# Kernel optimization log

Measured on AMD Instinct MI355X. Metric: run time of the kernel, lower is better.

Reference implementation:

```python
import jax, jax.numpy as jnp
import numpy as np

B, L, D, H, VOCAB = 8, 1024, 1024, 8, 32000
DH = D // H  # dim_per_head = 128
SCALE = float((DH // H) ** (-0.5))  # faithful to key.size(-1)//num_heads
EPS = 1e-5


def setup_inputs() -> dict:
    key = jax.random.key(0)
    ks = jax.random.split(key, 12)
    tokens = jax.random.randint(ks[0], (B, L), 0, VOCAB)
    s = 0.02
    emb = jax.random.normal(ks[1], (VOCAB, D), jnp.float32) * s
    emb = emb.at[0].set(0.0)  # padding_idx=0
    Wq = jax.random.normal(ks[2], (D, D), jnp.float32) * s
    Wk = jax.random.normal(ks[3], (D, D), jnp.float32) * s
    Wv = jax.random.normal(ks[4], (D, D), jnp.float32) * s
    Wo = jax.random.normal(ks[5], (D, D), jnp.float32) * s
    bq = jnp.zeros((D,), jnp.float32)
    bk = jnp.zeros((D,), jnp.float32)
    bv = jnp.zeros((D,), jnp.float32)
    bo = jnp.zeros((D,), jnp.float32)
    gamma = jnp.ones((2 * D,), jnp.float32)
    beta = jnp.zeros((2 * D,), jnp.float32)
    return {"tokens": tokens, "emb": emb, "Wq": Wq, "bq": bq, "Wk": Wk,
            "bk": bk, "Wv": Wv, "bv": bv, "Wo": Wo, "bo": bo,
            "gamma": gamma, "beta": beta}


def reference(tokens, emb, Wq, bq, Wk, bk, Wv, bv, Wo, bo, gamma, beta):
    # padding mask: [B, L, L] True where key token == 0
    pad = (tokens == 0)  # [B, L]
    mask = jnp.broadcast_to(pad[:, None, :], (B, L, L))
    mask = jnp.tile(mask, (H, 1, 1))  # torch .repeat(num_heads,1,1) -> [H*B, L, L]

    x = emb[tokens]  # [B, L, D]

    q = (x @ Wq + bq).reshape(B * H, L, DH)  # faithful interleaved view
    k = (x @ Wk + bk).reshape(B * H, L, DH)
    v = (x @ Wv + bv).reshape(B * H, L, DH)

    scores = jnp.einsum('bqd,bkd->bqk', q, k) * SCALE
    scores = jnp.where(mask, -jnp.inf, scores)
    attn = jax.nn.softmax(scores, axis=-1)
    ctx = jnp.einsum('bqk,bkd->bqd', attn, v).reshape(B, L, D)

    out = ctx @ Wo + bo  # [B, L, D]
    r = x + out
    maxpool = r.max(axis=1)   # [B, D]
    meanpool = r.mean(axis=1)  # [B, D]
    agg = jnp.concatenate([maxpool, meanpool], axis=1)  # [B, 2D]

    mu = agg.mean(axis=-1, keepdims=True)
    var = agg.var(axis=-1, keepdims=True)
    return (agg - mu) / jnp.sqrt(var + EPS) * gamma + beta
```

## Files before the change

### kernel.cpp

```cpp
#include <hip/hip_runtime.h>
#include <math.h>

typedef __attribute__((ext_vector_type(8))) short short8;
typedef __attribute__((ext_vector_type(4))) float f32x4;

constexpr int CB = 8, CL = 1024, CD = 1024, CDH = 128, CM = 8192;
constexpr float CSCALE = 0.25f;
constexpr float CEPS = 1e-5f;

__device__ inline ushort f2b(float f) {
    union { float f; unsigned u; } v; v.f = f;
    unsigned r = v.u + 0x7FFF + ((v.u >> 16) & 1);
    return (ushort)(r >> 16);
}

__device__ inline void gld16(const void* g, void* l) {
    __builtin_amdgcn_global_load_lds(
        (const __attribute__((address_space(1))) void*)g,
        (__attribute__((address_space(3))) void*)l, 16, 0, 0);
}

__global__ __launch_bounds__(256) void k_gather(const int* __restrict__ tokens,
                                                const float* __restrict__ emb,
                                                float* __restrict__ x,
                                                ushort* __restrict__ xb) {
    int row = blockIdx.x;
    int tok = tokens[row];
    float4 v = ((const float4*)(emb + (size_t)tok * CD))[threadIdx.x];
    ((float4*)(x + (size_t)row * CD))[threadIdx.x] = v;
    ushort4 o; o.x = f2b(v.x); o.y = f2b(v.y); o.z = f2b(v.z); o.w = f2b(v.w);
    ((ushort4*)(xb + (size_t)row * CD))[threadIdx.x] = o;
}

__global__ __launch_bounds__(256) void k_wtrans(const float* __restrict__ W,
                                                ushort* __restrict__ Wt) {
    __shared__ float ws_[32][33];
    const int tk = blockIdx.x * 32, tn = blockIdx.y * 32;
    const int t = threadIdx.x;
    {
        int r = t >> 3, c4 = (t & 7) * 4;
        *(float4*)&ws_[r][c4] = *(const float4*)&W[(size_t)(tk + r) * CD + tn + c4];
    }
    __syncthreads();
    int n = t >> 3, k4 = (t & 7) * 4;
    ushort4 o;
    o.x = f2b(ws_[k4 + 0][n]); o.y = f2b(ws_[k4 + 1][n]);
    o.z = f2b(ws_[k4 + 2][n]); o.w = f2b(ws_[k4 + 3][n]);
    *(ushort4*)&Wt[(size_t)(tn + n) * CD + tk + k4] = o;
}

__global__ __launch_bounds__(256) void k_gemm_qkv(const ushort* __restrict__ A,
                                                  const ushort* __restrict__ Wt3,
                                                  const float* __restrict__ b0,
                                                  const float* __restrict__ b1,
                                                  const float* __restrict__ b2,
                                                  ushort* __restrict__ C3) {
    __shared__ ushort As[128 * 32];
    __shared__ ushort Bs[128 * 32];
    const int z = blockIdx.z;
    const ushort* Bt  = Wt3 + (size_t)z * CD * CD;
    const float* bias = (z == 0) ? b0 : ((z == 1) ? b1 : b2);
    ushort* Cout      = C3 + (size_t)z * CM * CD;

    const int t = threadIdx.x, w = t >> 6, l = t & 63;
    const int lane15 = l & 15, quad = l >> 4;
    const int bm = blockIdx.y * 128, bn = blockIdx.x * 128;
    const int wm = (w >> 1) * 64, wn = (w & 1) * 64;
    const int arow = l >> 2;
    const int aseg = (l & 3) * 8;
    f32x4 acc[4][4] = {};

    for (int k0 = 0; k0 < CD; k0 += 32) {
        __syncthreads();
        #pragma unroll
        for (int c2 = 0; c2 < 2; ++c2) {
            int c = w * 2 + c2;
            gld16(A  + (size_t)(bm + c * 16 + arow) * CD + k0 + aseg, &As[c * 512 + l * 8]);
            gld16(Bt + (size_t)(bn + c * 16 + arow) * CD + k0 + aseg, &Bs[c * 512 + l * 8]);
        }
        __syncthreads();
        short8 af[4], bf[4];
        #pragma unroll
        for (int im = 0; im < 4; ++im)
            af[im] = *(const short8*)&As[(wm + im * 16 + lane15) * 32 + quad * 8];
        #pragma unroll
        for (int in = 0; in < 4; ++in)
            bf[in] = *(const short8*)&Bs[(wn + in * 16 + lane15) * 32 + quad * 8];
        #pragma unroll
        for (int im = 0; im < 4; ++im)
            #pragma unroll
            for (int in = 0; in < 4; ++in)
                acc[im][in] = __builtin_amdgcn_mfma_f32_16x16x32_bf16(af[im], bf[in], acc[im][in], 0, 0, 0);
    }
    #pragma unroll
    for (int in = 0; in < 4; ++in) {
        int col = bn + wn + in * 16 + lane15;
        float bv = bias[col];
        #pragma unroll
        for (int im = 0; im < 4; ++im) {
            int row0 = bm + wm + im * 16 + quad * 4;
            #pragma unroll
            for (int r = 0; r < 4; ++r)
                Cout[(size_t)(row0 + r) * CD + col] = f2b(acc[im][in][r] + bv);
        }
    }
}

__global__ __launch_bounds__(256) void k_gemm_out(const ushort* __restrict__ A,
                                                  const ushort* __restrict__ Bt,
                                                  const float* __restrict__ bias,
                                                  const float* __restrict__ resid,
                                                  float* __restrict__ Cout) {
    __shared__ ushort As[128 * 32];
    __shared__ ushort Bs[128 * 32];
    const int t = threadIdx.x, w = t >> 6, l = t & 63;
    const int lane15 = l & 15, quad = l >> 4;
    const int bm = blockIdx.y * 128, bn = blockIdx.x * 128;
    const int wm = (w >> 1) * 64, wn = (w & 1) * 64;
    const int arow = l >> 2;
    const int aseg = (l & 3) * 8;
    f32x4 acc[4][4] = {};

    for (int k0 = 0; k0 < CD; k0 += 32) {
        __syncthreads();
        #pragma unroll
        for (int c2 = 0; c2 < 2; ++c2) {
            int c = w * 2 + c2;
            gld16(A  + (size_t)(bm + c * 16 + arow) * CD + k0 + aseg, &As[c * 512 + l * 8]);
            gld16(Bt + (size_t)(bn + c * 16 + arow) * CD + k0 + aseg, &Bs[c * 512 + l * 8]);
        }
        __syncthreads();
        short8 af[4], bf[4];
        #pragma unroll
        for (int im = 0; im < 4; ++im)
            af[im] = *(const short8*)&As[(wm + im * 16 + lane15) * 32 + quad * 8];
        #pragma unroll
        for (int in = 0; in < 4; ++in)
            bf[in] = *(const short8*)&Bs[(wn + in * 16 + lane15) * 32 + quad * 8];
        #pragma unroll
        for (int im = 0; im < 4; ++im)
            #pragma unroll
            for (int in = 0; in < 4; ++in)
                acc[im][in] = __builtin_amdgcn_mfma_f32_16x16x32_bf16(af[im], bf[in], acc[im][in], 0, 0, 0);
    }
    #pragma unroll
    for (int in = 0; in < 4; ++in) {
        int col = bn + wn + in * 16 + lane15;
        float bv = bias[col];
        #pragma unroll
        for (int im = 0; im < 4; ++im) {
            int row0 = bm + wm + im * 16 + quad * 4;
            #pragma unroll
            for (int r = 0; r < 4; ++r) {
                size_t idx = (size_t)(row0 + r) * CD + col;
                Cout[idx] = acc[im][in][r] + bv + resid[idx];
            }
        }
    }
}

__global__ __launch_bounds__(256) void k_vtrans(const ushort* __restrict__ v,
                                                ushort* __restrict__ Vt) {
    __shared__ ushort Vs[16 * 1032];
    const int m0 = blockIdx.x * 16;
    const int i  = m0 >> 7;
    const int lb = (m0 & 127) * 8;
    const int t  = threadIdx.x;
    #pragma unroll
    for (int ii = 0; ii < 8; ++ii) {
        int vi = t + 256 * ii;
        int mm = vi >> 7, nv = vi & 127;
        *(uint4*)&Vs[mm * 1032 + nv * 8] = *(const uint4*)&v[(size_t)(m0 + mm) * CD + nv * 8];
    }
    __syncthreads();
    for (int oo = 0; oo < 64; ++oo) {
        int o = t + 256 * oo;
        int d = o >> 7, lpos = o & 127;
        int mm = lpos >> 3, c = lpos & 7;
        Vt[(size_t)i * (CDH * CL) + (size_t)d * CL + lb + lpos] = Vs[mm * 1032 + c * 128 + d];
    }
}

__global__ __launch_bounds__(256) void k_attn(const ushort* __restrict__ Q,
                                              const ushort* __restrict__ K,
                                              const ushort* __restrict__ Vt,
                                              const int* __restrict__ tokens,
                                              ushort* __restrict__ ctx) {
    __shared__ ushort Ks[16 * 512];
    __shared__ ushort Vs[16 * 512];
    __shared__ ushort Ps[4 * 1024];
    __shared__ float  Msk[CL];
    const int i = blockIdx.x, qb = blockIdx.y * 64;
    const int t = threadIdx.x, w = t >> 6, l = t & 63;
    const int lane15 = l & 15, quad = l >> 4;

    {
        const int* tokb = tokens + (i & 7) * CL;
        #pragma unroll
        for (int jj = 0; jj < 4; ++jj) {
            int idx = t + 256 * jj;
            Msk[idx] = (tokb[idx] == 0) ? -3.4e38f : 0.0f;
        }
    }
    const int qrow = qb + w * 16 + lane15;
    short8 af[4];
    #pragma unroll
    for (int kc = 0; kc < 4; ++kc)
        af[kc] = *(const short8*)&Q[(size_t)i * 131072 + (size_t)qrow * 128 + kc * 32 + quad * 8];

    f32x4 oacc[8];
    #pragma unroll
    for (int dt = 0; dt < 8; ++dt) oacc[dt] = f32x4{0.f, 0.f, 0.f, 0.f};
    float lsum[4] = {0.f, 0.f, 0.f, 0.f};
    const int wbase = w * 1024;

    for (int kt = 0; kt < 16; ++kt) {
        __syncthreads();
        #pragma unroll
        for (int s = 0; s < 4; ++s) {
            int p = w * 4 + s;
            gld16(K + (size_t)i * 131072 + (size_t)(kt * 64 + w * 16 + lane15) * 128 + (s * 4 + quad) * 8,
                  &Ks[p * 512 + l * 8]);
            int dt = p >> 1, ks2 = p & 1;
            gld16(Vt + (size_t)i * 131072 + (size_t)(dt * 16 + lane15) * 1024 + kt * 64 + (ks2 * 4 + quad) * 8,
                  &Vs[p * 512 + l * 8]);
        }
        __syncthreads();

        f32x4 sc[4];
        #pragma unroll
        for (int j = 0; j < 4; ++j) {
            sc[j] = f32x4{0.f, 0.f, 0.f, 0.f};
            #pragma unroll
            for (int kc = 0; kc < 4; ++kc) {
                short8 bk = *(const short8*)&Ks[(j * 4 + kc) * 512 + l * 8];
                sc[j] = __builtin_amdgcn_mfma_f32_16x16x32_bf16(af[kc], bk, sc[j], 0, 0, 0);
            }
        }
        #pragma unroll
        for (int j = 0; j < 4; ++j) {
            float mj = Msk[kt * 64 + j * 16 + lane15];
            #pragma unroll
            for (int r = 0; r < 4; ++r) {
                float p = __expf(fmaf(sc[j][r], CSCALE, mj));
                sc[j][r] = p;
                lsum[r] += p;
            }
        }
        #pragma unroll
        for (int j = 0; j < 4; ++j) {
            int ks2 = j >> 1;
            int qq  = (j & 1) * 2 + (lane15 >> 3);
            int pos = lane15 & 7;
            #pragma unroll
            for (int r = 0; r < 4; ++r)
                Ps[wbase + (ks2 * 64 + qq * 16 + quad * 4 + r) * 8 + pos] = f2b(sc[j][r]);
        }
        short8 ap[2];
        #pragma unroll
        for (int ks2 = 0; ks2 < 2; ++ks2)
            ap[ks2] = *(const short8*)&Ps[wbase + (ks2 * 64 + l) * 8];
        #pragma unroll
        for (int dt = 0; dt < 8; ++dt)
            #pragma unroll
            for (int ks2 = 0; ks2 < 2; ++ks2) {
                short8 bv = *(const short8*)&Vs[(dt * 2 + ks2) * 512 + l * 8];
                oacc[dt] = __builtin_amdgcn_mfma_f32_16x16x32_bf16(ap[ks2], bv, oacc[dt], 0, 0, 0);
            }
    }
    float inv[4];
    #pragma unroll
    for (int r = 0; r < 4; ++r) {
        float s = lsum[r];
        #pragma unroll
        for (int off = 1; off < 16; off <<= 1) s += __shfl_xor(s, off);
        inv[r] = 1.f / s;
    }
    #pragma unroll
    for (int dt = 0; dt < 8; ++dt)
        #pragma unroll
        for (int r = 0; r < 4; ++r) {
            int q = w * 16 + quad * 4 + r;
            ctx[(size_t)i * 131072 + (size_t)(qb + q) * 128 + dt * 16 + lane15] =
                f2b(oacc[dt][r] * inv[r]);
        }
}

__global__ __launch_bounds__(256) void k_pool1(const float* __restrict__ R,
                                               float* __restrict__ pmax,
                                               float* __restrict__ psum) {
    const int chunk = blockIdx.x, b = blockIdx.y;
    const int d4 = threadIdx.x;
    const float4* base = (const float4*)(R + ((size_t)b * CL + chunk * 32) * CD) + d4;
    float4 mx = base[0];
    float4 sm = mx;
    for (int lr = 1; lr < 32; ++lr) {
        float4 v = base[(size_t)lr * (CD / 4)];
        mx.x = fmaxf(mx.x, v.x); mx.y = fmaxf(mx.y, v.y);
        mx.z = fmaxf(mx.z, v.z); mx.w = fmaxf(mx.w, v.w);
        sm.x += v.x; sm.y += v.y; sm.z += v.z; sm.w += v.w;
    }
    size_t off = ((size_t)b * 32 + chunk) * CD;
    ((float4*)(pmax + off))[d4] = mx;
    ((float4*)(psum + off))[d4] = sm;
}

__global__ __launch_bounds__(1024) void k_pool2(const float* __restrict__ pmax,
                                                const float* __restrict__ psum,
                                                const float* __restrict__ gamma,
                                                const float* __restrict__ beta,
                                                float* __restrict__ out) {
    __shared__ float rs[16], rq[16];
    __shared__ float s_mu, s_inv;
    const int b = blockIdx.x;
    const int d = threadIdx.x;
    float mx = -3.4e38f, sm = 0.f;
    for (int c = 0; c < 32; ++c) {
        size_t off = ((size_t)b * 32 + c) * CD + d;
        mx = fmaxf(mx, pmax[off]);
        sm += psum[off];
    }
    const float a0 = mx;
    const float a1 = sm * (1.0f / 1024.0f);
    float s = a0 + a1;
    float qd = a0 * a0 + a1 * a1;
    #pragma unroll
    for (int off = 32; off > 0; off >>= 1) {
        s  += __shfl_xor(s, off);
        qd += __shfl_xor(qd, off);
    }
    const int wid = d >> 6;
    if ((d & 63) == 0) { rs[wid] = s; rq[wid] = qd; }
    __syncthreads();
    if (d == 0) {
        float S = 0.f, Qm = 0.f;
        for (int ww = 0; ww < 16; ++ww) { S += rs[ww]; Qm += rq[ww]; }
        float mu  = S * (1.0f / 2048.0f);
        float var = Qm * (1.0f / 2048.0f) - mu * mu;
        s_mu = mu; s_inv = 1.0f / sqrtf(var + CEPS);
    }
    __syncthreads();
    const float mu = s_mu, inv = s_inv;
    out[(size_t)b * 2048 + d]        = (a0 - mu) * inv * gamma[d]        + beta[d];
    out[(size_t)b * 2048 + 1024 + d] = (a1 - mu) * inv * gamma[1024 + d] + beta[1024 + d];
}

extern "C" void kernel_launch(void* const* d_in, const int* in_sizes, int n_in,
                              void* d_out, int out_size, void* d_ws, size_t ws_size,
                              hipStream_t stream) {
    const int*   tokens = (const int*)d_in[0];
    const float* emb    = (const float*)d_in[1];
    const float* Wq     = (const float*)d_in[2];
    const float* bq     = (const float*)d_in[3];
    const float* Wk     = (const float*)d_in[4];
    const float* bk     = (const float*)d_in[5];
    const float* Wv     = (const float*)d_in[6];
    const float* bv     = (const float*)d_in[7];
    const float* Wo     = (const float*)d_in[8];
    const float* bo     = (const float*)d_in[9];
    const float* gamma  = (const float*)d_in[10];
    const float* beta   = (const float*)d_in[11];
    float* out = (float*)d_out;

    char* p = (char*)d_ws;
    float*  x   = (float*)p;   p += (size_t)CM * CD * 4;
    ushort* xb  = (ushort*)p;  p += (size_t)CM * CD * 2;
    ushort* wqt = (ushort*)p;  p += (size_t)CD * CD * 2;
    ushort* wkt = (ushort*)p;  p += (size_t)CD * CD * 2;
    ushort* wvt = (ushort*)p;  p += (size_t)CD * CD * 2;
    ushort* wot = (ushort*)p;  p += (size_t)CD * CD * 2;
    ushort* qb_ = (ushort*)p;  p += (size_t)CM * CD * 2;
    ushort* kb_ = (ushort*)p;  p += (size_t)CM * CD * 2;
    ushort* vb_ = (ushort*)p;  p += (size_t)CM * CD * 2;
    ushort* Vt  = (ushort*)p;  p += (size_t)CM * CD * 2;
    float*  pmax = (float*)p;  p += (size_t)CB * 32 * CD * 4;
    float*  psum = (float*)p;  p += (size_t)CB * 32 * CD * 4;
    float*  R   = (float*)qb_;
    ushort* ctx = vb_;

    k_gather<<<CM, 256, 0, stream>>>(tokens, emb, x, xb);

    dim3 wg(32, 32);
    k_wtrans<<<wg, 256, 0, stream>>>(Wq, wqt);
    k_wtrans<<<wg, 256, 0, stream>>>(Wk, wkt);
    k_wtrans<<<wg, 256, 0, stream>>>(Wv, wvt);
    k_wtrans<<<wg, 256, 0, stream>>>(Wo, wot);

    dim3 gq(CD / 128, CM / 128, 3);
    k_gemm_qkv<<<gq, 256, 0, stream>>>(xb, wqt, bq, bk, bv, qb_);

    k_vtrans<<<CM / 16, 256, 0, stream>>>(vb_, Vt);

    dim3 ag(64, CL / 64);
    k_attn<<<ag, 256, 0, stream>>>(qb_, kb_, Vt, tokens, ctx);

    dim3 gg(CD / 128, CM / 128);
    k_gemm_out<<<gg, 256, 0, stream>>>(ctx, wot, bo, x, R);

    k_pool1<<<dim3(32, CB), 256, 0, stream>>>(R, pmax, psum);
    k_pool2<<<CB, 1024, 0, stream>>>(pmax, psum, gamma, beta, out);
}
```

Before: 424.4 us.

## Pre-pack V into MFMA tile layout and double query rows per attention block

```diff
diff --git a/kernel.cpp b/kernel.cpp
--- a/kernel.cpp
+++ b/kernel.cpp
@@ -12,6 +12,10 @@
     union { float f; unsigned u; } v; v.f = f;
     unsigned r = v.u + 0x7FFF + ((v.u >> 16) & 1);
     return (ushort)(r >> 16);
+}
+__device__ inline float b2f(ushort u) {
+    union { unsigned u; float f; } v; v.u = ((unsigned)u) << 16;
+    return v.f;
 }
 
 __device__ inline void gld16(const void* g, void* l) {
@@ -159,47 +163,58 @@
     }
 }
 
-__global__ __launch_bounds__(256) void k_vtrans(const ushort* __restrict__ v,
-                                                ushort* __restrict__ Vt) {
-    __shared__ ushort Vs[16 * 1032];
-    const int m0 = blockIdx.x * 16;
-    const int i  = m0 >> 7;
-    const int lb = (m0 & 127) * 8;
-    const int t  = threadIdx.x;
-    #pragma unroll
-    for (int ii = 0; ii < 8; ++ii) {
-        int vi = t + 256 * ii;
-        int mm = vi >> 7, nv = vi & 127;
-        *(uint4*)&Vs[mm * 1032 + nv * 8] = *(const uint4*)&v[(size_t)(m0 + mm) * CD + nv * 8];
+__global__ __launch_bounds__(256) void k_vtransp(const ushort* __restrict__ v,
+                                                 ushort* __restrict__ Vtp) {
+    __shared__ ushort Vs[64 * 136];
+    const int i = blockIdx.x >> 4, kt = blockIdx.x & 15;
+    const ushort* src = v + (size_t)i * 131072 + (size_t)kt * 64 * 128;
+    const int t = threadIdx.x;
+    #pragma unroll
+    for (int ii = 0; ii < 4; ++ii) {
+        int idx = t + 256 * ii;
+        int key = idx >> 4, seg = idx & 15;
+        *(uint4*)&Vs[key * 136 + seg * 8] = *(const uint4*)&src[key * 128 + seg * 8];
     }
     __syncthreads();
-    for (int oo = 0; oo < 64; ++oo) {
-        int o = t + 256 * oo;
-        int d = o >> 7, lpos = o & 127;
-        int mm = lpos >> 3, c = lpos & 7;
-        Vt[(size_t)i * (CDH * CL) + (size_t)d * CL + lb + lpos] = Vs[mm * 1032 + c * 128 + d];
-    }
-}
-
-__global__ __launch_bounds__(256) void k_attn(const ushort* __restrict__ Q,
+    ushort* dst = Vtp + (size_t)blockIdx.x * 8192;
+    #pragma unroll
+    for (int it = 0; it < 4; ++it) {
+        int L = t + 256 * it;
+        int cell = L & 63;
+        int quadk = cell >> 4, l15 = cell & 15;
+        int p = L >> 6;
+        int d = (p >> 1) * 16 + l15;
+        int kb = ((p & 1) * 4 + quadk) * 8;
+        uint pk[4];
+        #pragma unroll
+        for (int jj = 0; jj < 4; ++jj) {
+            uint lo = Vs[(kb + 2 * jj) * 136 + d];
+            uint hi = Vs[(kb + 2 * jj + 1) * 136 + d];
+            pk[jj] = lo | (hi << 16);
+        }
+        *(uint4*)&dst[(size_t)L * 8] = *(uint4*)pk;
+    }
+}
+
+__global__ __launch_bounds__(512) void k_attn(const ushort* __restrict__ Q,
                                               const ushort* __restrict__ K,
-                                              const ushort* __restrict__ Vt,
+                                              const ushort* __restrict__ Vtp,
                                               const int* __restrict__ tokens,
                                               ushort* __restrict__ ctx) {
     __shared__ ushort Ks[16 * 512];
     __shared__ ushort Vs[16 * 512];
-    __shared__ ushort Ps[4 * 1024];
-    __shared__ float  Msk[CL];
-    const int i = blockIdx.x, qb = blockIdx.y * 64;
+    __shared__ ushort Ps[8 * 1088];
+    __shared__ ushort Msk[CL];
+    const int i = blockIdx.x, qb = blockIdx.y * 128;
     const int t = threadIdx.x, w = t >> 6, l = t & 63;
     const int lane15 = l & 15, quad = l >> 4;
 
     {
         const int* tokb = tokens + (i & 7) * CL;
         #pragma unroll
-        for (int jj = 0; jj < 4; ++jj) {
-            int idx = t + 256 * jj;
-            Msk[idx] = (tokb[idx] == 0) ? -3.4e38f : 0.0f;
+        for (int jj = 0; jj < 2; ++jj) {
+            int idx = t + 512 * jj;
+            Msk[idx] = (tokb[idx] == 0) ? (ushort)0xFF80 : (ushort)0;
         }
     }
     const int qrow = qb + w * 16 + lane15;
@@ -212,17 +227,17 @@
     #pragma unroll
     for (int dt = 0; dt < 8; ++dt) oacc[dt] = f32x4{0.f, 0.f, 0.f, 0.f};
     float lsum[4] = {0.f, 0.f, 0.f, 0.f};
-    const int wbase = w * 1024;
+    const int wbase = w * 1088;
 
     for (int kt = 0; kt < 16; ++kt) {
         __syncthreads();
         #pragma unroll
-        for (int s = 0; s < 4; ++s) {
-            int p = w * 4 + s;
-            gld16(K + (size_t)i * 131072 + (size_t)(kt * 64 + w * 16 + lane15) * 128 + (s * 4 + quad) * 8,
+        for (int c = 0; c < 2; ++c) {
+            int p = w * 2 + c;
+            gld16(K + (size_t)i * 131072 + (size_t)(kt * 64 + (p >> 2) * 16 + lane15) * 128
+                    + (p & 3) * 32 + quad * 8,
                   &Ks[p * 512 + l * 8]);
-            int dt = p >> 1, ks2 = p & 1;
-            gld16(Vt + (size_t)i * 131072 + (size_t)(dt * 16 + lane15) * 1024 + kt * 64 + (ks2 * 4 + quad) * 8,
+            gld16(Vtp + ((size_t)(i * 16 + kt) * 16 + p) * 512 + l * 8,
                   &Vs[p * 512 + l * 8]);
         }
         __syncthreads();
@@ -239,7 +254,7 @@
         }
         #pragma unroll
         for (int j = 0; j < 4; ++j) {
-            float mj = Msk[kt * 64 + j * 16 + lane15];
+            float mj = b2f(Msk[kt * 64 + j * 16 + lane15]);
             #pragma unroll
             for (int r = 0; r < 4; ++r) {
                 float p = __expf(fmaf(sc[j][r], CSCALE, mj));
@@ -253,13 +268,16 @@
             int qq  = (j & 1) * 2 + (lane15 >> 3);
             int pos = lane15 & 7;
             #pragma unroll
-            for (int r = 0; r < 4; ++r)
-                Ps[wbase + (ks2 * 64 + qq * 16 + quad * 4 + r) * 8 + pos] = f2b(sc[j][r]);
+            for (int r = 0; r < 4; ++r) {
+                union { float f; unsigned u; } cv; cv.f = sc[j][r];
+                Ps[wbase + ks2 * 544 + qq * 136 + (quad * 4 + r) * 8 + pos] =
+                    (ushort)(cv.u >> 16);
+            }
         }
         short8 ap[2];
         #pragma unroll
         for (int ks2 = 0; ks2 < 2; ++ks2)
-            ap[ks2] = *(const short8*)&Ps[wbase + (ks2 * 64 + l) * 8];
+            ap[ks2] = *(const short8*)&Ps[wbase + ks2 * 544 + quad * 136 + lane15 * 8];
         #pragma unroll
         for (int dt = 0; dt < 8; ++dt)
             #pragma unroll
@@ -280,8 +298,8 @@
     for (int dt = 0; dt < 8; ++dt)
         #pragma unroll
         for (int r = 0; r < 4; ++r) {
-            int q = w * 16 + quad * 4 + r;
-            ctx[(size_t)i * 131072 + (size_t)(qb + q) * 128 + dt * 16 + lane15] =
+            int q = qb + w * 16 + quad * 4 + r;
+            ctx[(size_t)i * 131072 + (size_t)q * 128 + dt * 16 + lane15] =
                 f2b(oacc[dt][r] * inv[r]);
         }
 }
@@ -372,7 +390,7 @@
     ushort* qb_ = (ushort*)p;  p += (size_t)CM * CD * 2;
     ushort* kb_ = (ushort*)p;  p += (size_t)CM * CD * 2;
     ushort* vb_ = (ushort*)p;  p += (size_t)CM * CD * 2;
-    ushort* Vt  = (ushort*)p;  p += (size_t)CM * CD * 2;
+    ushort* Vtp = (ushort*)p;  p += (size_t)CM * CD * 2;
     float*  pmax = (float*)p;  p += (size_t)CB * 32 * CD * 4;
     float*  psum = (float*)p;  p += (size_t)CB * 32 * CD * 4;
     float*  R   = (float*)qb_;
@@ -389,10 +407,10 @@
     dim3 gq(CD / 128, CM / 128, 3);
     k_gemm_qkv<<<gq, 256, 0, stream>>>(xb, wqt, bq, bk, bv, qb_);
 
-    k_vtrans<<<CM / 16, 256, 0, stream>>>(vb_, Vt);
-
-    dim3 ag(64, CL / 64);
-    k_attn<<<ag, 256, 0, stream>>>(qb_, kb_, Vt, tokens, ctx);
+    k_vtransp<<<64 * 16, 256, 0, stream>>>(vb_, Vtp);
+
+    dim3 ag(64, 8);
+    k_attn<<<ag, 512, 0, stream>>>(qb_, kb_, Vtp, tokens, ctx);
 
     dim3 gg(CD / 128, CM / 128);
     k_gemm_out<<<gg, 256, 0, stream>>>(ctx, wot, bo, x, R);
```

Result: faster. 382.1 us (-10.0%).
